# Kernel tuning notes

Hardware: AMD Instinct MI355X
Metric: run time of the kernel (lower is better)

Reference implementation:

```python
import jax, jax.numpy as jnp
import numpy as np

B, N, H = 32, 256, 1024
HEADS, NHID = 8, 128
NCLS = 7
BAND = 24
ALPHA = 0.2          # GAT leaky-relu slope
NEG = -9e15          # masked-attention fill, as in pyGAT


def setup_inputs() -> dict:
    key = jax.random.key(0)
    ks = jax.random.split(key, 16)
    def nrm(k, shp, s=0.02):
        return jax.random.normal(k, shp, dtype=jnp.float32) * s
    hidden_cls = jax.random.normal(ks[0], (B, N, H), dtype=jnp.float32)
    hidden_emo = jax.random.normal(ks[1], (B, N, H), dtype=jnp.float32)
    # causal band cliques, diagonal included (GAT uses clique - eye)
    t = jnp.arange(N)
    band = ((t[None, :] <= t[:, None]) & (t[None, :] > t[:, None] - BAND)).astype(jnp.float32)
    clique = jnp.broadcast_to(band, (B, N, N))
    labels = jax.random.randint(ks[2], (B, N), 0, NCLS)
    pooler_W = nrm(ks[3], (H, H)); pooler_b = jnp.zeros((H,), jnp.float32)
    gat_W = nrm(ks[4], (HEADS, H, NHID))
    gat_a1 = nrm(ks[5], (HEADS, NHID)); gat_a2 = nrm(ks[6], (HEADS, NHID))
    out_W = nrm(ks[7], (H, H))            # heads*nhid == H -> nclass=H
    out_a1 = nrm(ks[8], (H,)); out_a2 = nrm(ks[9], (H,))
    lin1_W = nrm(ks[10], (H, H)); lin1_b = jnp.zeros((H,), jnp.float32)
    lin0_W = nrm(ks[11], (2 * H, H)); lin0_b = jnp.zeros((H,), jnp.float32)
    cls_W = nrm(ks[12], (H, NCLS)); cls_b = jnp.zeros((NCLS,), jnp.float32)
    A = jax.random.uniform(ks[13], (NCLS, NCLS), dtype=jnp.float32) + 0.1
    hmm_A = A / A.sum(axis=1, keepdims=True)   # row-stochastic transition matrix
    return dict(hidden_cls=hidden_cls, hidden_emo=hidden_emo, clique=clique,
                labels=labels, pooler_W=pooler_W, pooler_b=pooler_b,
                gat_W=gat_W, gat_a1=gat_a1, gat_a2=gat_a2,
                out_W=out_W, out_a1=out_a1, out_a2=out_a2,
                lin1_W=lin1_W, lin1_b=lin1_b, lin0_W=lin0_W, lin0_b=lin0_b,
                cls_W=cls_W, cls_b=cls_b, hmm_A=hmm_A)


def _lrelu(x):
    return jnp.where(x > 0, x, ALPHA * x)


def reference(hidden_cls, hidden_emo, clique, labels, pooler_W, pooler_b,
              gat_W, gat_a1, gat_a2, out_W, out_a1, out_a2,
              lin1_W, lin1_b, lin0_W, lin0_b, cls_W, cls_b, hmm_A):
    # PoolerAll: dense + tanh on all token states (dropout = identity in eval)
    fea_cls = jnp.tanh(hidden_cls @ pooler_W + pooler_b)   # [B,N,H] (CLS per utt)
    fea_emo = jnp.tanh(hidden_emo @ pooler_W + pooler_b)   # [B,N,H] (mask tok per utt)

    eyeN = jnp.eye(N, dtype=clique.dtype)
    adjm = (clique - eyeN) > 0                             # [B,N,N] GAT adjacency

    def gat_one(x, am):                                    # x [N,H], am [N,N]
        Wh = jnp.einsum('nf,hfd->hnd', x, gat_W)           # [heads,N,nhid]
        e = _lrelu(jnp.einsum('hnd,hd->hn', Wh, gat_a1)[:, :, None]
                   + jnp.einsum('hnd,hd->hn', Wh, gat_a2)[:, None, :])
        att = jax.nn.softmax(jnp.where(am[None], e, NEG), axis=-1)
        h1 = jax.nn.elu(jnp.einsum('hnm,hmd->hnd', att, Wh))
        h1 = jnp.transpose(h1, (1, 0, 2)).reshape(N, HEADS * NHID)
        Wh2 = h1 @ out_W                                   # out attention layer (concat=False)
        e2 = _lrelu((Wh2 @ out_a1)[:, None] + (Wh2 @ out_a2)[None, :])
        h2 = jax.nn.softmax(jnp.where(am, e2, NEG), axis=-1) @ Wh2
        return jax.nn.elu(h2)                              # [N,H]

    gat_out = jax.vmap(gat_one)(fea_cls, adjm)             # [B,N,H]
    # row 0 replaced by (dropout of) fea_cls row 0, as in the original
    g = jnp.concatenate([fea_cls[:, :1], gat_out[:, 1:]], axis=1)
    g = jnp.concatenate([fea_cls, g @ lin1_W + lin1_b], axis=-1) @ lin0_W + lin0_b
    log_gat = jax.nn.softmax(g @ cls_W + cls_b, axis=-1)   # [B,N,NCLS] (probs)

    # HMM emission probs hmm_B(fea) = softmax(classifier(fea))
    Bprob = jax.nn.softmax(fea_emo @ cls_W + cls_b, axis=-1)  # [B,N,NCLS]
    P0 = jnp.full((NCLS,), 1.0 / NCLS, dtype=jnp.float32)
    AT = hmm_A.T

    def hmm_row(Bp, mrow):                                 # Bp [N,NCLS], mrow [N]
        def step(carry, xs):
            p, started = carry
            bt, m = xs
            p_init = P0 * bt; p_init = p_init / p_init.sum()
            p_tr = (AT @ p) * bt; p_tr = p_tr / p_tr.sum()
            p_new = jnp.where(started, p_tr, p_init)
            valid = m > 0.5
            return (jnp.where(valid, p_new, p), started | valid), None
        (p, _), _ = jax.lax.scan(step, (P0, jnp.asarray(False)), (Bp, mrow))
        return p                                           # final filtered posterior

    log_hmm = jax.vmap(lambda Bp, M: jax.vmap(lambda mr: hmm_row(Bp, mr))(M))(Bprob, clique)

    logits = jnp.log((log_gat + log_hmm) * 0.5).reshape(B * N, NCLS)
    lab = labels.reshape(B * N)
    mask = lab >= 0
    picked = jnp.take_along_axis(logits, jnp.where(mask, lab, 0)[:, None], axis=1)[:, 0]
    loss = -(jnp.where(mask, picked, 0.0).sum() / jnp.maximum(mask.sum(), 1).astype(jnp.float32))
    return loss, logits
```

## Files before the change

kernel.cpp:

```cpp
#include <hip/hip_runtime.h>
#include <hip/hip_bf16.h>
#include <math.h>

typedef __hip_bfloat16 bf16;
typedef __attribute__((ext_vector_type(8))) short short8;
typedef __attribute__((ext_vector_type(4))) float float4v;

static constexpr int Bb = 32, Nn = 256, Hh = 1024, HEADS = 8, NHID = 128, NCLS = 7, BAND = 24;
static constexpr int M = Bb * Nn;
static constexpr float ALPHA = 0.2f;
static constexpr long INEL = (long)M * Hh;

__device__ __forceinline__ float tof(bf16 x) { return __bfloat162float(x); }
__device__ __forceinline__ bf16 tob(float x) { return __float2bfloat16(x); }
__device__ __forceinline__ unsigned short f2bits(float x) {
    bf16 h = __float2bfloat16(x);
    return *(unsigned short*)&h;
}
__device__ __forceinline__ float bits2f(unsigned short u) {
    unsigned v = ((unsigned)u) << 16;
    float f;
    __builtin_memcpy(&f, &v, 4);
    return f;
}

__device__ __forceinline__ void gload16(const void* g, void* l) {
    __builtin_amdgcn_global_load_lds(
        (const __attribute__((address_space(1))) void*)g,
        (__attribute__((address_space(3))) void*)l, 16, 0, 0);
}

static constexpr long OFF_PWT  = 0;
static constexpr long OFF_PB   = 1048576;
static constexpr long OFF_WCT  = 1049600;
static constexpr long OFF_GA1  = 2098176;
static constexpr long OFF_GA2  = 2099200;
static constexpr long OFF_OWT  = 2100224;
static constexpr long OFF_OA1  = 3148800;
static constexpr long OFF_OA2  = 3149824;
static constexpr long OFF_L1WT = 3150848;
static constexpr long OFF_L1B  = 4199424;
static constexpr long OFF_L0WT = 4200448;
static constexpr long OFF_L0B  = 6297600;
static constexpr long OFF_CWT  = 6298624;
static constexpr long OFF_CB   = 6305792;
static constexpr long OFF_HA   = 6305799;
static constexpr long W_TOTAL  = 6305848;

__global__ void probe_k(const void* __restrict__ p, int* __restrict__ flag) {
    int t = threadIdx.x;
    int bad = 0;
    for (int i = t; i < 4096; i += 256) {
        float v = tof(((const bf16*)p)[i]);
        if (!(fabsf(v) < 1e4f)) bad = 1;
    }
    __shared__ int sb[256];
    sb[t] = bad; __syncthreads();
    for (int s = 128; s; s >>= 1) { if (t < s) sb[t] |= sb[t + s]; __syncthreads(); }
    if (t == 0) *flag = sb[0] ? 0 : 1;
}

__device__ __forceinline__ float ldany(const void* p, long i, int isb) {
    return isb ? tof(((const bf16*)p)[i]) : ((const float*)p)[i];
}

__global__ void convert_k(const int* __restrict__ flagp,
                          const void* pW, const void* pb, const void* gW,
                          const void* ga1, const void* ga2, const void* oW,
                          const void* oa1, const void* oa2, const void* l1W,
                          const void* l1b, const void* l0W, const void* l0b,
                          const void* cW, const void* cb, const void* hA,
                          bf16* __restrict__ dst) {
    long idx = (long)blockIdx.x * 256 + threadIdx.x;
    if (idx >= W_TOTAL) return;
    int isb = *flagp;
    const void* src; long si;
    if      (idx < OFF_PB)   { long l = idx;            long n = l >> 10, k = l & 1023;
                               src = pW;  si = k * 1024 + n; }
    else if (idx < OFF_WCT)  { src = pb;  si = idx - OFF_PB; }
    else if (idx < OFF_GA1)  { long l = idx - OFF_WCT;  long n = l >> 10, f = l & 1023;
                               long h = n >> 7, d = n & 127;
                               src = gW;  si = h * 131072 + f * 128 + d; }
    else if (idx < OFF_GA2)  { src = ga1; si = idx - OFF_GA1; }
    else if (idx < OFF_OWT)  { src = ga2; si = idx - OFF_GA2; }
    else if (idx < OFF_OA1)  { long l = idx - OFF_OWT;  long n = l >> 10, k = l & 1023;
                               src = oW;  si = k * 1024 + n; }
    else if (idx < OFF_OA2)  { src = oa1; si = idx - OFF_OA1; }
    else if (idx < OFF_L1WT) { src = oa2; si = idx - OFF_OA2; }
    else if (idx < OFF_L1B)  { long l = idx - OFF_L1WT; long n = l >> 10, k = l & 1023;
                               src = l1W; si = k * 1024 + n; }
    else if (idx < OFF_L0WT) { src = l1b; si = idx - OFF_L1B; }
    else if (idx < OFF_L0B)  { long l = idx - OFF_L0WT; long n = l >> 11, k = l & 2047;
                               src = l0W; si = k * 1024 + n; }
    else if (idx < OFF_CWT)  { src = l0b; si = idx - OFF_L0B; }
    else if (idx < OFF_CB)   { long l = idx - OFF_CWT;  long c = l >> 10, k = l & 1023;
                               src = cW;  si = k * 7 + c; }
    else if (idx < OFF_HA)   { src = cb;  si = idx - OFF_CB; }
    else                     { src = hA;  si = idx - OFF_HA; }
    dst[idx] = tob(ldany(src, si, isb));
}

__global__ void convin_k(const int* __restrict__ flagp, const void* __restrict__ s0,
                         const void* __restrict__ s1, bf16* __restrict__ d0,
                         bf16* __restrict__ d1) {
    const int isb = *flagp;
    long i = ((long)blockIdx.x * 256 + threadIdx.x) * 8;
    const void* s; bf16* d; long off;
    if (i < INEL) { s = s0; d = d0; off = i; }
    else          { s = s1; d = d1; off = i - INEL; }
    if (isb) {
        *(int4*)(d + off) = *(const int4*)((const bf16*)s + off);
    } else {
        const float* f = (const float*)s + off;
        unsigned short tmp[8];
        #pragma unroll
        for (int q = 0; q < 8; ++q) tmp[q] = f2bits(f[q]);
        *(int4*)(d + off) = *(int4*)tmp;
    }
}

template <int ACT>
__device__ __forceinline__ void gemm_core(const bf16* __restrict__ A,
                                          const bf16* __restrict__ Bt,
                                          const bf16* __restrict__ bias,
                                          bf16* __restrict__ Cout,
                                          unsigned short* As, unsigned short* Bs,
                                          int Nc, int K, int bm, int bn) {
    const int tid = threadIdx.x;
    const int lane = tid & 63;
    const int wave = tid >> 6;
    const int wm = (wave >> 1) * 64, wn = (wave & 1) * 64;
    const int l15 = lane & 15, quad = lane >> 4;
    const int r0 = wave * 32;
    const int lrow = lane >> 2, lchunk = (lane & 3) * 8;

    float4v acc[4][4];
    #pragma unroll
    for (int i = 0; i < 4; ++i)
        #pragma unroll
        for (int j = 0; j < 4; ++j) acc[i][j] = (float4v){0.f, 0.f, 0.f, 0.f};

    const bf16* ga = A + (long)(bm + r0 + lrow) * K + lchunk;
    const bf16* gb = Bt + (long)(bn + r0 + lrow) * K + lchunk;
    for (int k0 = 0; k0 < K; k0 += 32) {
        gload16(ga + k0, As + r0 * 32);
        gload16(ga + (long)16 * K + k0, As + (r0 + 16) * 32);
        gload16(gb + k0, Bs + r0 * 32);
        gload16(gb + (long)16 * K + k0, Bs + (r0 + 16) * 32);
        __syncthreads();
        short8 af[4], bfr[4];
        #pragma unroll
        for (int i = 0; i < 4; ++i) af[i] = *(const short8*)(As + (wm + i * 16 + l15) * 32 + quad * 8);
        #pragma unroll
        for (int j = 0; j < 4; ++j) bfr[j] = *(const short8*)(Bs + (wn + j * 16 + l15) * 32 + quad * 8);
        #pragma unroll
        for (int i = 0; i < 4; ++i)
            #pragma unroll
            for (int j = 0; j < 4; ++j)
                acc[i][j] = __builtin_amdgcn_mfma_f32_16x16x32_bf16(af[i], bfr[j], acc[i][j], 0, 0, 0);
        __syncthreads();
    }
    #pragma unroll
    for (int j = 0; j < 4; ++j) {
        int gn = bn + wn + j * 16 + l15;
        float bj = bias ? tof(bias[gn]) : 0.f;
        #pragma unroll
        for (int i = 0; i < 4; ++i) {
            #pragma unroll
            for (int r = 0; r < 4; ++r) {
                int gm = bm + wm + i * 16 + quad * 4 + r;
                float v = acc[i][j][r] + bj;
                if (ACT == 1) v = tanhf(v);
                Cout[(long)gm * Nc + gn] = tob(v);
            }
        }
    }
}

template <int ACT>
__global__ __launch_bounds__(256) void gemm_fast_k(const bf16* __restrict__ A,
                                                   const bf16* __restrict__ Bt,
                                                   const bf16* __restrict__ bias,
                                                   bf16* __restrict__ Cout,
                                                   int Nc, int K) {
    __shared__ unsigned short As[128 * 32];
    __shared__ unsigned short Bs[128 * 32];
    gemm_core<ACT>(A, Bt, bias, Cout, As, Bs, Nc, K, blockIdx.x * 128, blockIdx.y * 128);
}

__global__ __launch_bounds__(256) void gemmP_k(const bf16* __restrict__ A0,
                                               const bf16* __restrict__ A1,
                                               const bf16* __restrict__ Bt,
                                               const bf16* __restrict__ bias,
                                               bf16* __restrict__ C0,
                                               bf16* __restrict__ C1) {
    __shared__ unsigned short As[128 * 32];
    __shared__ unsigned short Bs[128 * 32];
    const bf16* A = blockIdx.z ? A1 : A0;
    bf16* C = blockIdx.z ? C1 : C0;
    gemm_core<1>(A, Bt, bias, C, As, Bs, Hh, Hh, blockIdx.x * 128, blockIdx.y * 128);
}

__global__ __launch_bounds__(256) void gemm2_fast_k(const bf16* __restrict__ A1,
                                                    const bf16* __restrict__ A2,
                                                    const bf16* __restrict__ Bt,
                                                    const bf16* __restrict__ bias,
                                                    bf16* __restrict__ Cout) {
    constexpr int Nc = 1024, K = 2048;
    __shared__ unsigned short As[128 * 32];
    __shared__ unsigned short Bs[128 * 32];
    const int tid = threadIdx.x;
    const int lane = tid & 63;
    const int wave = tid >> 6;
    const int wm = (wave >> 1) * 64, wn = (wave & 1) * 64;
    const int l15 = lane & 15, quad = lane >> 4;
    const int r0 = wave * 32;
    const int lrow = lane >> 2, lchunk = (lane & 3) * 8;
    const int bm = blockIdx.x * 128, bn = blockIdx.y * 128;

    float4v acc[4][4];
    #pragma unroll
    for (int i = 0; i < 4; ++i)
        #pragma unroll
        for (int j = 0; j < 4; ++j) acc[i][j] = (float4v){0.f, 0.f, 0.f, 0.f};

    const bf16* gb = Bt + (long)(bn + r0 + lrow) * K + lchunk;
    for (int k0 = 0; k0 < K; k0 += 32) {
        const bf16* Asrc = (k0 < 1024) ? A1 : A2;
        int kl = k0 & 1023;
        const bf16* ga = Asrc + (long)(bm + r0 + lrow) * 1024 + kl + lchunk;
        gload16(ga, As + r0 * 32);
        gload16(ga + 16 * 1024, As + (r0 + 16) * 32);
        gload16(gb + k0, Bs + r0 * 32);
        gload16(gb + (long)16 * K + k0, Bs + (r0 + 16) * 32);
        __syncthreads();
        short8 af[4], bfr[4];
        #pragma unroll
        for (int i = 0; i < 4; ++i) af[i] = *(const short8*)(As + (wm + i * 16 + l15) * 32 + quad * 8);
        #pragma unroll
        for (int j = 0; j < 4; ++j) bfr[j] = *(const short8*)(Bs + (wn + j * 16 + l15) * 32 + quad * 8);
        #pragma unroll
        for (int i = 0; i < 4; ++i)
            #pragma unroll
            for (int j = 0; j < 4; ++j)
                acc[i][j] = __builtin_amdgcn_mfma_f32_16x16x32_bf16(af[i], bfr[j], acc[i][j], 0, 0, 0);
        __syncthreads();
    }
    #pragma unroll
    for (int j = 0; j < 4; ++j) {
        int gn = bn + wn + j * 16 + l15;
        float bj = tof(bias[gn]);
        #pragma unroll
        for (int i = 0; i < 4; ++i)
            #pragma unroll
            for (int r = 0; r < 4; ++r) {
                int gm = bm + wm + i * 16 + quad * 4 + r;
                Cout[(long)gm * Nc + gn] = tob(acc[i][j][r] + bj);
            }
    }
}

__global__ __launch_bounds__(256) void att1f_k(const bf16* __restrict__ Wh,
                                               const bf16* __restrict__ ga1,
                                               const bf16* __restrict__ ga2,
                                               bf16* __restrict__ h1) {
    __shared__ unsigned short S[152][128];
    __shared__ float f1s[152], f2s[152];
    __shared__ float att[128][25];
    const int bx = blockIdx.x;
    const int b = bx >> 4, h = (bx >> 1) & 7, half = bx & 1;
    const int nbase = half * 128;
    const int mstart = half ? (nbase - (BAND - 1)) : 0;
    const int mcount = half ? (256 - mstart) : 128;
    const int t = threadIdx.x;
    const int c = t & 15;

    float av1[8], av2[8];
    {
        union { int4 v; unsigned short us[8]; } u1, u2;
        u1.v = *(const int4*)(ga1 + h * 128 + c * 8);
        u2.v = *(const int4*)(ga2 + h * 128 + c * 8);
        #pragma unroll
        for (int q = 0; q < 8; ++q) { av1[q] = bits2f(u1.us[q]); av2[q] = bits2f(u2.us[q]); }
    }

    const int iters = (mcount * 16 + 255) >> 8;
    for (int i = 0; i < iters; ++i) {
        int li = i * 256 + t;
        int mr = li >> 4;
        if (mr < mcount) {
            long ga = (long)(b * 256 + mstart + mr) * 1024 + h * 128 + c * 8;
            union { int4 v; unsigned short us[8]; } u;
            u.v = *(const int4*)(Wh + ga);
            float p1 = 0.f, p2 = 0.f;
            #pragma unroll
            for (int q = 0; q < 8; ++q) {
                float f = bits2f(u.us[q]);
                p1 += f * av1[q]; p2 += f * av2[q];
            }
            *(int4*)&S[mr][c * 8] = u.v;
            #pragma unroll
            for (int mask = 1; mask < 16; mask <<= 1) {
                p1 += __shfl_xor(p1, mask);
                p2 += __shfl_xor(p2, mask);
            }
            if (c == 0) { f1s[mr] = p1; f2s[mr] = p2; }
        }
    }
    __syncthreads();

    if (t < 128) {
        int n = nbase + t;
        if (n > 0) {
            int cnt = n < (BAND - 1) ? n : (BAND - 1);
            int m0 = n - cnt;
            float f1n = f1s[n - mstart];
            float e[BAND - 1];
            float mx = -1e30f;
            for (int i = 0; i < cnt; ++i) {
                float v = f1n + f2s[m0 + i - mstart];
                v = v > 0.f ? v : ALPHA * v;
                e[i] = v; mx = fmaxf(mx, v);
            }
            float ss = 0.f;
            for (int i = 0; i < cnt; ++i) { e[i] = __expf(e[i] - mx); ss += e[i]; }
            float inv = 1.0f / ss;
            for (int i = 0; i < cnt; ++i) att[t][i] = e[i] * inv;
        }
    }
    __syncthreads();

    const int wave = t >> 6, lane = t & 63;
    for (int ln = wave; ln < 128; ln += 4) {
        int n = nbase + ln;
        if (n == 0) continue;
        int cnt = n < (BAND - 1) ? n : (BAND - 1);
        int mr0 = n - cnt - mstart;
        float s0 = 0.f, s1 = 0.f;
        for (int i = 0; i < cnt; ++i) {
            float a = att[ln][i];
            unsigned u = *(const unsigned*)&S[mr0 + i][lane * 2];
            s0 += a * bits2f((unsigned short)(u & 0xffff));
            s1 += a * bits2f((unsigned short)(u >> 16));
        }
        s0 = s0 > 0.f ? s0 : expm1f(s0);
        s1 = s1 > 0.f ? s1 : expm1f(s1);
        unsigned out = (unsigned)f2bits(s0) | ((unsigned)f2bits(s1) << 16);
        *(unsigned*)(h1 + (long)(b * 256 + n) * 1024 + h * 128 + lane * 2) = out;
    }
}

__global__ void mean1_k(const bf16* __restrict__ Wh, bf16* __restrict__ h1) {
    int bh = blockIdx.x;
    int h = bh & 7, b = bh >> 3;
    int lane = threadIdx.x;
    float s0 = 0.f, s1 = 0.f;
    long base = (long)(b * 256) * 1024 + h * 128 + lane * 2;
    for (int m = 0; m < 256; ++m) {
        unsigned u = *(const unsigned*)(Wh + base + (long)m * 1024);
        s0 += bits2f((unsigned short)(u & 0xffff));
        s1 += bits2f((unsigned short)(u >> 16));
    }
    s0 *= (1.0f / 256.0f); s1 *= (1.0f / 256.0f);
    s0 = s0 > 0.f ? s0 : expm1f(s0);
    s1 = s1 > 0.f ? s1 : expm1f(s1);
    unsigned out = (unsigned)f2bits(s0) | ((unsigned)f2bits(s1) << 16);
    *(unsigned*)(h1 + base) = out;
}

__global__ void f12b_k(const bf16* __restrict__ Wh2, const bf16* __restrict__ a1,
                       const bf16* __restrict__ a2, float* __restrict__ f1b,
                       float* __restrict__ f2b) {
    int idx = blockIdx.x;
    int lane = threadIdx.x;
    const bf16* row = Wh2 + (long)idx * 1024 + lane * 16;
    float s1 = 0.f, s2 = 0.f;
    #pragma unroll
    for (int half = 0; half < 2; ++half) {
        union { int4 v; unsigned short us[8]; } x, w1, w2;
        x.v  = *(const int4*)(row + half * 8);
        w1.v = *(const int4*)(a1 + lane * 16 + half * 8);
        w2.v = *(const int4*)(a2 + lane * 16 + half * 8);
        #pragma unroll
        for (int q = 0; q < 8; ++q) {
            float f = bits2f(x.us[q]);
            s1 += f * bits2f(w1.us[q]);
            s2 += f * bits2f(w2.us[q]);
        }
    }
    #pragma unroll
    for (int off = 32; off; off >>= 1) {
        s1 += __shfl_down(s1, off);
        s2 += __shfl_down(s2, off);
    }
    if (lane == 0) { f1b[idx] = s1; f2b[idx] = s2; }
}

__global__ __launch_bounds__(256) void att2f_k(const bf16* __restrict__ Wh2,
                                               const float* __restrict__ f1b,
                                               const float* __restrict__ f2b,
                                               bf16* __restrict__ g) {
    __shared__ unsigned short S[152][128];
    __shared__ float att[128][25];
    const int bx = blockIdx.x;
    const int b = bx >> 4, half = (bx >> 3) & 1, jt = bx & 7;
    const int nbase = half * 128;
    const int mstart = half ? (nbase - (BAND - 1)) : 0;
    const int mcount = half ? (256 - mstart) : 128;
    const int t = threadIdx.x;
    const int c = t & 15;

    const int iters = (mcount * 16 + 255) >> 8;
    for (int i = 0; i < iters; ++i) {
        int li = i * 256 + t;
        int mr = li >> 4;
        if (mr < mcount) {
            long ga = (long)(b * 256 + mstart + mr) * 1024 + jt * 128 + c * 8;
            *(int4*)&S[mr][c * 8] = *(const int4*)(Wh2 + ga);
        }
    }
    __syncthreads();

    if (t < 128) {
        int n = nbase + t;
        if (n > 0) {
            int cnt = n < (BAND - 1) ? n : (BAND - 1);
            int m0 = n - cnt;
            float f1n = f1b[b * 256 + n];
            float e[BAND - 1];
            float mx = -1e30f;
            for (int i = 0; i < cnt; ++i) {
                float v = f1n + f2b[b * 256 + m0 + i];
                v = v > 0.f ? v : ALPHA * v;
                e[i] = v; mx = fmaxf(mx, v);
            }
            float ss = 0.f;
            for (int i = 0; i < cnt; ++i) { e[i] = __expf(e[i] - mx); ss += e[i]; }
            float inv = 1.0f / ss;
            for (int i = 0; i < cnt; ++i) att[t][i] = e[i] * inv;
        }
    }
    __syncthreads();

    const int wave = t >> 6, lane = t & 63;
    for (int ln = wave; ln < 128; ln += 4) {
        int n = nbase + ln;
        if (n == 0) continue;
        int cnt = n < (BAND - 1) ? n : (BAND - 1);
        int mr0 = n - cnt - mstart;
        float s0 = 0.f, s1 = 0.f;
        for (int i = 0; i < cnt; ++i) {
            float a = att[ln][i];
            unsigned u = *(const unsigned*)&S[mr0 + i][lane * 2];
            s0 += a * bits2f((unsigned short)(u & 0xffff));
            s1 += a * bits2f((unsigned short)(u >> 16));
        }
        s0 = s0 > 0.f ? s0 : expm1f(s0);
        s1 = s1 > 0.f ? s1 : expm1f(s1);
        unsigned out = (unsigned)f2bits(s0) | ((unsigned)f2bits(s1) << 16);
        *(unsigned*)(g + (long)(b * 256 + n) * 1024 + jt * 128 + lane * 2) = out;
    }
}

__global__ void g_row0_k(const bf16* __restrict__ fea_cls, bf16* __restrict__ g) {
    int b = blockIdx.x;
    int t = threadIdx.x;
    long base = (long)(b * 256) * 1024 + t * 8;
    *(int4*)(g + base) = *(const int4*)(fea_cls + base);
}

__global__ void cls7_k(const bf16* __restrict__ X, const bf16* __restrict__ Wt,
                       const bf16* __restrict__ b, float* __restrict__ out, int K) {
    int row = blockIdx.x;
    int lane = threadIdx.x;
    float xv[16];
    {
        const bf16* x = X + (long)row * K + lane * 16;
        union { int4 v; unsigned short us[8]; } u0, u1;
        u0.v = *(const int4*)x; u1.v = *(const int4*)(x + 8);
        #pragma unroll
        for (int q = 0; q < 8; ++q) { xv[q] = bits2f(u0.us[q]); xv[q + 8] = bits2f(u1.us[q]); }
    }
    float acc[NCLS];
    #pragma unroll
    for (int cc = 0; cc < NCLS; ++cc) {
        const bf16* wr = Wt + (long)cc * K + lane * 16;
        union { int4 v; unsigned short us[8]; } w0, w1;
        w0.v = *(const int4*)wr; w1.v = *(const int4*)(wr + 8);
        float s = 0.f;
        #pragma unroll
        for (int q = 0; q < 8; ++q) {
            s += xv[q] * bits2f(w0.us[q]);
            s += xv[q + 8] * bits2f(w1.us[q]);
        }
        acc[cc] = s;
    }
    #pragma unroll
    for (int cc = 0; cc < NCLS; ++cc)
        #pragma unroll
        for (int off = 32; off; off >>= 1) acc[cc] += __shfl_down(acc[cc], off);
    if (lane == 0) {
        float mx = -1e30f;
        #pragma unroll
        for (int cc = 0; cc < NCLS; ++cc) { acc[cc] += tof(b[cc]); mx = fmaxf(mx, acc[cc]); }
        float s = 0.f;
        #pragma unroll
        for (int cc = 0; cc < NCLS; ++cc) { acc[cc] = expf(acc[cc] - mx); s += acc[cc]; }
        float inv = 1.0f / s;
        #pragma unroll
        for (int cc = 0; cc < NCLS; ++cc) out[(long)row * NCLS + cc] = acc[cc] * inv;
    }
}

__global__ void hmm_k(const float* __restrict__ Bprob, const bf16* __restrict__ hmm_A,
                      float* __restrict__ out) {
    __shared__ float AT[NCLS][NCLS];
    int t = threadIdx.x;
    if (t < NCLS * NCLS) {
        int i = t / NCLS, j = t % NCLS;
        AT[i][j] = tof(hmm_A[j * NCLS + i]);
    }
    __syncthreads();
    int idx = blockIdx.x * blockDim.x + t;
    int n = idx & 255, b = idx >> 8;
    int t0 = n - (BAND - 1) > 0 ? n - (BAND - 1) : 0;
    const float* Bp = Bprob + (long)(b * 256) * NCLS;
    float p[NCLS];
    float s = 0.f;
    #pragma unroll
    for (int cc = 0; cc < NCLS; ++cc) { p[cc] = Bp[t0 * NCLS + cc]; s += p[cc]; }
    float inv = 1.0f / s;
    #pragma unroll
    for (int cc = 0; cc < NCLS; ++cc) p[cc] *= inv;
    for (int tt = t0 + 1; tt <= n; ++tt) {
        float q[NCLS]; float ss = 0.f;
        #pragma unroll
        for (int i = 0; i < NCLS; ++i) {
            float a = 0.f;
            #pragma unroll
            for (int j = 0; j < NCLS; ++j) a += AT[i][j] * p[j];
            a *= Bp[tt * NCLS + i];
            q[i] = a; ss += a;
        }
        float iv = 1.0f / ss;
        #pragma unroll
        for (int i = 0; i < NCLS; ++i) p[i] = q[i] * iv;
    }
    #pragma unroll
    for (int cc = 0; cc < NCLS; ++cc) out[(long)idx * NCLS + cc] = p[cc];
}

__global__ void zero_k(float* p) { *p = 0.f; }

__global__ void final_k(const float* __restrict__ lg, const float* __restrict__ lh,
                        const int* __restrict__ labels, void* __restrict__ out,
                        float* __restrict__ loss_acc, const int* __restrict__ flagp) {
    int idx = blockIdx.x * blockDim.x + threadIdx.x;
    const int isb = *flagp;
    float lo[NCLS];
    int lab = labels[idx];
    #pragma unroll
    for (int c = 0; c < NCLS; ++c) {
        float v = logf(0.5f * (lg[(long)idx * NCLS + c] + lh[(long)idx * NCLS + c]));
        lo[c] = v;
        long o = 1 + (long)idx * NCLS + c;
        if (isb) ((bf16*)out)[o] = tob(v);
        else     ((float*)out)[o] = v;
    }
    float picked = lo[lab];
    __shared__ float red[256];
    red[threadIdx.x] = picked;
    __syncthreads();
    for (int s = 128; s; s >>= 1) {
        if (threadIdx.x < s) red[threadIdx.x] += red[threadIdx.x + s];
        __syncthreads();
    }
    if (threadIdx.x == 0) atomicAdd(loss_acc, red[0]);
}

__global__ void loss_k(const float* __restrict__ acc, void* __restrict__ out,
                       const int* __restrict__ flagp) {
    float v = -acc[0] / (float)(Bb * Nn);
    if (*flagp) ((bf16*)out)[0] = tob(v);
    else        ((float*)out)[0] = v;
}

extern "C" void kernel_launch(void* const* d_in, const int* in_sizes, int n_in,
                              void* d_out, int out_size, void* d_ws, size_t ws_size,
                              hipStream_t stream) {
    const void* hidden_cls = d_in[0];
    const void* hidden_emo = d_in[1];
    const int* labels = (const int*)d_in[3];

    char* w = (char*)d_ws;
    bf16* C  = (bf16*)w;
    bf16* E  = C + INEL;
    bf16* Wb = E + INEL;
    bf16* H2 = Wb + INEL;
    bf16* wc = H2 + INEL;
    float* f1b   = (float*)(wc + W_TOTAL);
    float* f2b   = f1b + M;
    float* Bprob = f2b + M;
    float* lgat  = Bprob + (long)M * NCLS;
    float* lhmm  = lgat + (long)M * NCLS;
    float* loss_acc = lhmm + (long)M * NCLS;
    int*   flag  = (int*)(loss_acc + 1);

    dim3 gblk(256);
    dim3 ggrid(M / 128, Hh / 128);
    dim3 pgrid(M / 128, Hh / 128, 2);

    probe_k<<<1, 256, 0, stream>>>(d_in[4], flag);
    convert_k<<<(int)((W_TOTAL + 255) / 256), 256, 0, stream>>>(
        flag, d_in[4], d_in[5], d_in[6], d_in[7], d_in[8], d_in[9], d_in[10],
        d_in[11], d_in[12], d_in[13], d_in[14], d_in[15], d_in[16], d_in[17],
        d_in[18], wc);
    convin_k<<<(int)(2 * INEL / (256 * 8)), 256, 0, stream>>>(flag, hidden_emo, hidden_cls, Wb, H2);

    gemmP_k<<<pgrid, gblk, 0, stream>>>(Wb, H2, wc + OFF_PWT, wc + OFF_PB, E, C);
    cls7_k<<<M, 64, 0, stream>>>(E, wc + OFF_CWT, wc + OFF_CB, Bprob, Hh);
    gemm_fast_k<0><<<ggrid, gblk, 0, stream>>>(C, wc + OFF_WCT, (const bf16*)nullptr, Wb, Hh, Hh);
    att1f_k<<<512, 256, 0, stream>>>(Wb, wc + OFF_GA1, wc + OFF_GA2, E);
    mean1_k<<<Bb * HEADS, 64, 0, stream>>>(Wb, E);
    gemm_fast_k<0><<<ggrid, gblk, 0, stream>>>(E, wc + OFF_OWT, (const bf16*)nullptr, Wb, Hh, Hh);
    f12b_k<<<M, 64, 0, stream>>>(Wb, wc + OFF_OA1, wc + OFF_OA2, f1b, f2b);
    g_row0_k<<<Bb, 128, 0, stream>>>(C, E);
    att2f_k<<<512, 256, 0, stream>>>(Wb, f1b, f2b, E);
    gemm_fast_k<0><<<ggrid, gblk, 0, stream>>>(E, wc + OFF_L1WT, wc + OFF_L1B, Wb, Hh, Hh);
    gemm2_fast_k<<<ggrid, gblk, 0, stream>>>(C, Wb, wc + OFF_L0WT, wc + OFF_L0B, E);
    cls7_k<<<M, 64, 0, stream>>>(E, wc + OFF_CWT, wc + OFF_CB, lgat, Hh);
    hmm_k<<<M / 256, 256, 0, stream>>>(Bprob, wc + OFF_HA, lhmm);
    zero_k<<<1, 1, 0, stream>>>(loss_acc);
    final_k<<<M / 256, 256, 0, stream>>>(lgat, lhmm, labels, d_out, loss_acc, flag);
    loss_k<<<1, 1, 0, stream>>>(loss_acc, d_out, flag);
}
```

Before: 511.1 us.

## Swizzle GEMM LDS layout and double the K-step per barrier pair

```diff
diff --git a/kernel.cpp b/kernel.cpp
--- a/kernel.cpp
+++ b/kernel.cpp
@@ -132,7 +132,11 @@
     const int wm = (wave >> 1) * 64, wn = (wave & 1) * 64;
     const int l15 = lane & 15, quad = lane >> 4;
     const int r0 = wave * 32;
-    const int lrow = lane >> 2, lchunk = (lane & 3) * 8;
+    const int lrow = lane >> 2, q = lane & 3;
+    const int rA = r0 + lrow, rB = r0 + 16 + lrow;
+    const int qa = (q ^ (rA & 3) ^ ((rA >> 2) & 3)) * 8;
+    const int qb = (q ^ (rB & 3) ^ ((rB >> 2) & 3)) * 8;
+    const int sc8 = (quad ^ (l15 & 3) ^ (l15 >> 2)) * 8;
 
     float4v acc[4][4];
     #pragma unroll
@@ -140,24 +144,38 @@
         #pragma unroll
         for (int j = 0; j < 4; ++j) acc[i][j] = (float4v){0.f, 0.f, 0.f, 0.f};
 
-    const bf16* ga = A + (long)(bm + r0 + lrow) * K + lchunk;
-    const bf16* gb = Bt + (long)(bn + r0 + lrow) * K + lchunk;
-    for (int k0 = 0; k0 < K; k0 += 32) {
-        gload16(ga + k0, As + r0 * 32);
-        gload16(ga + (long)16 * K + k0, As + (r0 + 16) * 32);
-        gload16(gb + k0, Bs + r0 * 32);
-        gload16(gb + (long)16 * K + k0, Bs + (r0 + 16) * 32);
+    const bf16* ga0 = A + (long)(bm + rA) * K + qa;
+    const bf16* ga1 = A + (long)(bm + rB) * K + qb;
+    const bf16* gb0 = Bt + (long)(bn + rA) * K + qa;
+    const bf16* gb1 = Bt + (long)(bn + rB) * K + qb;
+
+    for (int k0 = 0; k0 < K; k0 += 64) {
+        gload16(ga0 + k0,      As + r0 * 32);
+        gload16(ga1 + k0,      As + (r0 + 16) * 32);
+        gload16(ga0 + k0 + 32, As + 4096 + r0 * 32);
+        gload16(ga1 + k0 + 32, As + 4096 + (r0 + 16) * 32);
+        gload16(gb0 + k0,      Bs + r0 * 32);
+        gload16(gb1 + k0,      Bs + (r0 + 16) * 32);
+        gload16(gb0 + k0 + 32, Bs + 4096 + r0 * 32);
+        gload16(gb1 + k0 + 32, Bs + 4096 + (r0 + 16) * 32);
         __syncthreads();
-        short8 af[4], bfr[4];
-        #pragma unroll
-        for (int i = 0; i < 4; ++i) af[i] = *(const short8*)(As + (wm + i * 16 + l15) * 32 + quad * 8);
-        #pragma unroll
-        for (int j = 0; j < 4; ++j) bfr[j] = *(const short8*)(Bs + (wn + j * 16 + l15) * 32 + quad * 8);
-        #pragma unroll
-        for (int i = 0; i < 4; ++i)
+        #pragma unroll
+        for (int ks = 0; ks < 2; ++ks) {
+            const unsigned short* Au = As + ks * 4096;
+            const unsigned short* Bu = Bs + ks * 4096;
+            short8 af[4], bfr[4];
+            #pragma unroll
+            for (int i = 0; i < 4; ++i)
+                af[i] = *(const short8*)(Au + (wm + i * 16 + l15) * 32 + sc8);
             #pragma unroll
             for (int j = 0; j < 4; ++j)
-                acc[i][j] = __builtin_amdgcn_mfma_f32_16x16x32_bf16(af[i], bfr[j], acc[i][j], 0, 0, 0);
+                bfr[j] = *(const short8*)(Bu + (wn + j * 16 + l15) * 32 + sc8);
+            #pragma unroll
+            for (int i = 0; i < 4; ++i)
+                #pragma unroll
+                for (int j = 0; j < 4; ++j)
+                    acc[i][j] = __builtin_amdgcn_mfma_f32_16x16x32_bf16(af[i], bfr[j], acc[i][j], 0, 0, 0);
+        }
         __syncthreads();
     }
     #pragma unroll
@@ -183,8 +201,8 @@
                                                    const bf16* __restrict__ bias,
                                                    bf16* __restrict__ Cout,
                                                    int Nc, int K) {
-    __shared__ unsigned short As[128 * 32];
-    __shared__ unsigned short Bs[128 * 32];
+    __shared__ unsigned short As[2 * 128 * 32];
+    __shared__ unsigned short Bs[2 * 128 * 32];
     gemm_core<ACT>(A, Bt, bias, Cout, As, Bs, Nc, K, blockIdx.x * 128, blockIdx.y * 128);
 }
 
@@ -194,8 +212,8 @@
                                                const bf16* __restrict__ bias,
                                                bf16* __restrict__ C0,
                                                bf16* __restrict__ C1) {
-    __shared__ unsigned short As[128 * 32];
-    __shared__ unsigned short Bs[128 * 32];
+    __shared__ unsigned short As[2 * 128 * 32];
+    __shared__ unsigned short Bs[2 * 128 * 32];
     const bf16* A = blockIdx.z ? A1 : A0;
     bf16* C = blockIdx.z ? C1 : C0;
     gemm_core<1>(A, Bt, bias, C, As, Bs, Hh, Hh, blockIdx.x * 128, blockIdx.y * 128);
@@ -207,15 +225,19 @@
                                                     const bf16* __restrict__ bias,
                                                     bf16* __restrict__ Cout) {
     constexpr int Nc = 1024, K = 2048;
-    __shared__ unsigned short As[128 * 32];
-    __shared__ unsigned short Bs[128 * 32];
+    __shared__ unsigned short As[2 * 128 * 32];
+    __shared__ unsigned short Bs[2 * 128 * 32];
     const int tid = threadIdx.x;
     const int lane = tid & 63;
     const int wave = tid >> 6;
     const int wm = (wave >> 1) * 64, wn = (wave & 1) * 64;
     const int l15 = lane & 15, quad = lane >> 4;
     const int r0 = wave * 32;
-    const int lrow = lane >> 2, lchunk = (lane & 3) * 8;
+    const int lrow = lane >> 2, q = lane & 3;
+    const int rA = r0 + lrow, rB = r0 + 16 + lrow;
+    const int qa = (q ^ (rA & 3) ^ ((rA >> 2) & 3)) * 8;
+    const int qb = (q ^ (rB & 3) ^ ((rB >> 2) & 3)) * 8;
+    const int sc8 = (quad ^ (l15 & 3) ^ (l15 >> 2)) * 8;
     const int bm = blockIdx.x * 128, bn = blockIdx.y * 128;
 
     float4v acc[4][4];
@@ -224,26 +246,39 @@
         #pragma unroll
         for (int j = 0; j < 4; ++j) acc[i][j] = (float4v){0.f, 0.f, 0.f, 0.f};
 
-    const bf16* gb = Bt + (long)(bn + r0 + lrow) * K + lchunk;
-    for (int k0 = 0; k0 < K; k0 += 32) {
+    const bf16* gb0 = Bt + (long)(bn + rA) * K + qa;
+    const bf16* gb1 = Bt + (long)(bn + rB) * K + qb;
+    for (int k0 = 0; k0 < K; k0 += 64) {
         const bf16* Asrc = (k0 < 1024) ? A1 : A2;
         int kl = k0 & 1023;
-        const bf16* ga = Asrc + (long)(bm + r0 + lrow) * 1024 + kl + lchunk;
-        gload16(ga, As + r0 * 32);
-        gload16(ga + 16 * 1024, As + (r0 + 16) * 32);
-        gload16(gb + k0, Bs + r0 * 32);
-        gload16(gb + (long)16 * K + k0, Bs + (r0 + 16) * 32);
+        const bf16* ga0 = Asrc + (long)(bm + rA) * 1024 + kl + qa;
+        const bf16* ga1 = Asrc + (long)(bm + rB) * 1024 + kl + qb;
+        gload16(ga0,      As + r0 * 32);
+        gload16(ga1,      As + (r0 + 16) * 32);
+        gload16(ga0 + 32, As + 4096 + r0 * 32);
+        gload16(ga1 + 32, As + 4096 + (r0 + 16) * 32);
+        gload16(gb0 + k0,      Bs + r0 * 32);
+        gload16(gb1 + k0,      Bs + (r0 + 16) * 32);
+        gload16(gb0 + k0 + 32, Bs + 4096 + r0 * 32);
+        gload16(gb1 + k0 + 32, Bs + 4096 + (r0 + 16) * 32);
         __syncthreads();
-        short8 af[4], bfr[4];
-        #pragma unroll
-        for (int i = 0; i < 4; ++i) af[i] = *(const short8*)(As + (wm + i * 16 + l15) * 32 + quad * 8);
-        #pragma unroll
-        for (int j = 0; j < 4; ++j) bfr[j] = *(const short8*)(Bs + (wn + j * 16 + l15) * 32 + quad * 8);
-        #pragma unroll
-        for (int i = 0; i < 4; ++i)
+        #pragma unroll
+        for (int ks = 0; ks < 2; ++ks) {
+            const unsigned short* Au = As + ks * 4096;
+            const unsigned short* Bu = Bs + ks * 4096;
+            short8 af[4], bfr[4];
+            #pragma unroll
+            for (int i = 0; i < 4; ++i)
+                af[i] = *(const short8*)(Au + (wm + i * 16 + l15) * 32 + sc8);
             #pragma unroll
             for (int j = 0; j < 4; ++j)
-                acc[i][j] = __builtin_amdgcn_mfma_f32_16x16x32_bf16(af[i], bfr[j], acc[i][j], 0, 0, 0);
+                bfr[j] = *(const short8*)(Bu + (wn + j * 16 + l15) * 32 + sc8);
+            #pragma unroll
+            for (int i = 0; i < 4; ++i)
+                #pragma unroll
+                for (int j = 0; j < 4; ++j)
+                    acc[i][j] = __builtin_amdgcn_mfma_f32_16x16x32_bf16(af[i], bfr[j], acc[i][j], 0, 0, 0);
+        }
         __syncthreads();
     }
     #pragma unroll
@@ -281,7 +316,7 @@
         u1.v = *(const int4*)(ga1 + h * 128 + c * 8);
         u2.v = *(const int4*)(ga2 + h * 128 + c * 8);
         #pragma unroll
-        for (int q = 0; q < 8; ++q) { av1[q] = bits2f(u1.us[q]); av2[q] = bits2f(u2.us[q]); }
+        for (int qq = 0; qq < 8; ++qq) { av1[qq] = bits2f(u1.us[qq]); av2[qq] = bits2f(u2.us[qq]); }
     }
 
     const int iters = (mcount * 16 + 255) >> 8;
@@ -294,9 +329,9 @@
             u.v = *(const int4*)(Wh + ga);
             float p1 = 0.f, p2 = 0.f;
             #pragma unroll
-            for (int q = 0; q < 8; ++q) {
-                float f = bits2f(u.us[q]);
-                p1 += f * av1[q]; p2 += f * av2[q];
+            for (int qq = 0; qq < 8; ++qq) {
+                float f = bits2f(u.us[qq]);
+                p1 += f * av1[qq]; p2 += f * av2[qq];
             }
             *(int4*)&S[mr][c * 8] = u.v;
             #pragma unroll
```

Result: faster. 488.5 us (-4.4%).
